# Kernel optimization log

Measured on AMD Instinct MI355X. Metric: run time of the kernel, lower is better.

## Reference

```python
import jax, jax.numpy as jnp
import numpy as np

T, B, L, I, H = 1024, 1024, 10, 10, 10


def setup_inputs() -> dict:
    key = jax.random.key(0)
    ks = jax.random.split(key, 7)
    scale = 1.0 / np.sqrt(H)
    x = jax.random.normal(ks[0], (T, B, I), dtype=jnp.float32)
    hp = jax.random.normal(ks[1], (L, B, H), dtype=jnp.float32)
    cp = jax.random.normal(ks[2], (L, B, H), dtype=jnp.float32)
    # torch nn.LSTM params, uniform(-1/sqrt(H), 1/sqrt(H)); layer 0 input = I == H so all layers stack
    W_ih = jax.random.uniform(ks[3], (L, 4 * H, I), minval=-scale, maxval=scale, dtype=jnp.float32)
    W_hh = jax.random.uniform(ks[4], (L, 4 * H, H), minval=-scale, maxval=scale, dtype=jnp.float32)
    b_ih = jax.random.uniform(ks[5], (L, 4 * H), minval=-scale, maxval=scale, dtype=jnp.float32)
    b_hh = jax.random.uniform(ks[6], (L, 4 * H), minval=-scale, maxval=scale, dtype=jnp.float32)
    return {"x": x, "hp": hp, "cp": cp, "W_ih": W_ih, "W_hh": W_hh, "b_ih": b_ih, "b_hh": b_hh}


def _run_layer(inp, h0, c0, Wi, Wh, bi, bh):
    # precompute input projections for all timesteps: [T, B, 4H]
    xg = jnp.einsum('tbi,gi->tbg', inp, Wi) + bi + bh

    def step(carry, xg_t):
        h, c = carry
        g = xg_t + h @ Wh.T  # [B, 4H]; torch gate order: i, f, g, o
        i_g, f_g, g_g, o_g = jnp.split(g, 4, axis=-1)
        i_g = jax.nn.sigmoid(i_g)
        f_g = jax.nn.sigmoid(f_g)
        g_g = jnp.tanh(g_g)
        o_g = jax.nn.sigmoid(o_g)
        c = f_g * c + i_g * g_g
        h = o_g * jnp.tanh(c)
        return (h, c), h

    (hT, cT), ys = jax.lax.scan(step, (h0, c0), xg)
    return ys, hT, cT


def reference(x, hp, cp, W_ih, W_hh, b_ih, b_hh):
    out = x
    hns, cns = [], []
    for l in range(hp.shape[0]):  # fixed small layer stack
        out, hn, cn = _run_layer(out, hp[l], cp[l], W_ih[l], W_hh[l], b_ih[l], b_hh[l])
        hns.append(hn)
        cns.append(cn)
    return out, jnp.stack(hns), jnp.stack(cns)
```

## Files before the change

kernel.cpp:

```cpp
#include <hip/hip_runtime.h>

namespace {

constexpr int T = 1024;
constexpr int B = 1024;
constexpr int L = 10;
constexpr int H = 10;
constexpr int NTHREADS = 128;
constexpr int U = 4;
constexpr int NWIN = T / U;
constexpr int NINT = NWIN + L - 1;
constexpr int BH = B * H;
constexpr int ROWP = 12;

using v2f = __attribute__((ext_vector_type(2))) float;
using v4f = __attribute__((ext_vector_type(4))) float;

__device__ __forceinline__ v2f v2fma(v2f a, v2f b, v2f c) {
    return __builtin_elementwise_fma(a, b, c);
}
__device__ __forceinline__ void pin2(v2f& v) { asm volatile("" : "+v"(v)); }
__device__ __forceinline__ float rcp_f(float x) { return __builtin_amdgcn_rcpf(x); }
__device__ __forceinline__ float exp2_f(float x) {
    float r; asm("v_exp_f32 %0, %1" : "=v"(r) : "v"(x)); return r;
}
__device__ __forceinline__ v2f lo2(v4f q) { return __builtin_shufflevector(q, q, 0, 1); }
__device__ __forceinline__ v2f hi2(v4f q) { return __builtin_shufflevector(q, q, 2, 3); }
#define LDS_FENCE asm volatile("" ::: "memory")

__global__
__attribute__((amdgpu_flat_work_group_size(NTHREADS, NTHREADS)))
__attribute__((amdgpu_waves_per_eu(2)))
void lstm_pipeline(const float* __restrict__ x,
                   const float* __restrict__ hp,
                   const float* __restrict__ cp,
                   const float* __restrict__ Wih,
                   const float* __restrict__ Whh,
                   const float* __restrict__ bih,
                   const float* __restrict__ bhh,
                   float* __restrict__ out,
                   float* __restrict__ hn,
                   float* __restrict__ cn)
{
    __shared__ __align__(16) float buf[2][U][L + 1][ROWP];

    const int tid = threadIdx.x;
    const int wv = tid >> 6;
    const int ln = tid & 63;
    int lidx;
    if (wv == 0) lidx = (ln < 60) ? ln : (ln - 10);
    else         lidx = (ln < 40) ? (60 + ln) : (90 + (ln - 40) % 10);
    const int l = lidx / 10;
    const int j = lidx % 10;
    const int b = blockIdx.x;
    const int boff = b * H + j;

    const float NL2E = -1.44269504088896340736f;
    v2f wi[4][5], wh[4][5], bias[4];
    {
        const float* WiL = Wih + (size_t)l * 4 * H * H;
        const float* WhL = Whh + (size_t)l * 4 * H * H;
        const int bo = l * 4 * H;
        #pragma unroll
        for (int g = 0; g < 4; ++g) {
            const float s = (g == 2) ? 2.0f * NL2E : NL2E;
            const float* wr = WiL + (size_t)(g * H + j) * H;
            const float* hr = WhL + (size_t)(g * H + j) * H;
            #pragma unroll
            for (int p = 0; p < 5; ++p) {
                wi[g][p][0] = wr[2 * p] * s; wi[g][p][1] = wr[2 * p + 1] * s;
                wh[g][p][0] = hr[2 * p] * s; wh[g][p][1] = hr[2 * p + 1] * s;
            }
            bias[g][0] = (bih[bo + g * H + j] + bhh[bo + g * H + j]) * s;
            bias[g][1] = 0.0f;
        }
    }
    #pragma unroll
    for (int g = 0; g < 4; ++g) {
        #pragma unroll
        for (int p = 0; p < 5; ++p) { pin2(wi[g][p]); pin2(wh[g][p]); }
        pin2(bias[g]);
    }

    float h = hp[(l * B + b) * H + j];
    float c = cp[(l * B + b) * H + j];
    buf[(l + 1) & 1][U - 1][l + 1][j] = h;

    const bool is_st = (lidx < 10);
    float xcur[U], xnext[U];
    if (is_st) {
        #pragma unroll
        for (int u = 0; u < U; ++u)
            buf[1][u][0][j] = x[(size_t)u * BH + boff];
        #pragma unroll
        for (int u = 0; u < U; ++u) xcur[u] = x[(size_t)(U + u) * BH + boff];
    }
    __syncthreads();

    v2f acc[U][4];

    auto prefetchx = [&](int k) {
        if (is_st && (k + 2) < NWIN) {
            #pragma unroll
            for (int u = 0; u < U; ++u)
                xnext[u] = x[(size_t)((k + 2) * U + u) * BH + boff];
        }
    };

    auto phase1 = [&](int k, int rp) {
        const unsigned w = (unsigned)(k - l);
        if (w < (unsigned)NWIN) {
            #pragma unroll
            for (int u = 0; u < U; ++u) {
                const float* xr = &buf[rp][u][l][0];
                v4f q0 = *(const v4f*)(xr + 0);
                v4f q1 = *(const v4f*)(xr + 4);
                v2f q2 = *(const v2f*)(xr + 8);
                #pragma unroll
                for (int g = 0; g < 4; ++g) {
                    v2f a = v2fma(wi[g][0], lo2(q0), bias[g]);
                    a = v2fma(wi[g][1], hi2(q0), a);
                    a = v2fma(wi[g][2], lo2(q1), a);
                    a = v2fma(wi[g][3], hi2(q1), a);
                    a = v2fma(wi[g][4], q2, a);
                    acc[u][g] = a;
                }
            }
        }
    };

    auto phase2 = [&](int k, int wp, int rp) {
        const unsigned w = (unsigned)(k - l);
        if (w < (unsigned)NWIN) {
            const float* hr0 = &buf[rp][U - 1][l + 1][0];
            v4f hq0 = *(const v4f*)(hr0 + 0);
            v4f hq1 = *(const v4f*)(hr0 + 4);
            v2f hq2 = *(const v2f*)(hr0 + 8);
            float hv[U];
            #pragma unroll
            for (int u = 0; u < U; ++u) {
                v4f q0, q1; v2f q2;
                if (u == 0) { q0 = hq0; q1 = hq1; q2 = hq2; }
                else {
                    const float* hr = &buf[wp][u - 1][l + 1][0];
                    q0 = *(const v4f*)(hr + 0);
                    q1 = *(const v4f*)(hr + 4);
                    q2 = *(const v2f*)(hr + 8);
                }
                v2f aI = v2fma(wh[0][0], lo2(q0), acc[u][0]);
                v2f aF = v2fma(wh[1][0], lo2(q0), acc[u][1]);
                v2f aG = v2fma(wh[2][0], lo2(q0), acc[u][2]);
                v2f aO = v2fma(wh[3][0], lo2(q0), acc[u][3]);
                aI = v2fma(wh[0][1], hi2(q0), aI);
                aF = v2fma(wh[1][1], hi2(q0), aF);
                aG = v2fma(wh[2][1], hi2(q0), aG);
                aO = v2fma(wh[3][1], hi2(q0), aO);
                aI = v2fma(wh[0][2], lo2(q1), aI);
                aF = v2fma(wh[1][2], lo2(q1), aF);
                aG = v2fma(wh[2][2], lo2(q1), aG);
                aO = v2fma(wh[3][2], lo2(q1), aO);
                aI = v2fma(wh[0][3], hi2(q1), aI);
                aF = v2fma(wh[1][3], hi2(q1), aF);
                aG = v2fma(wh[2][3], hi2(q1), aG);
                aO = v2fma(wh[3][3], hi2(q1), aO);
                aI = v2fma(wh[0][4], q2, aI);
                aF = v2fma(wh[1][4], q2, aF);
                aG = v2fma(wh[2][4], q2, aG);
                aO = v2fma(wh[3][4], q2, aO);
                const float pI = aI[0] + aI[1];
                const float pF = aF[0] + aF[1];
                const float pG = aG[0] + aG[1];
                const float pO = aO[0] + aO[1];
                const float Ei = exp2_f(pI);
                const float Ef = exp2_f(pF);
                const float Eg = exp2_f(pG);
                const float Eo = exp2_f(pO);
                const float d1 = 1.0f + Ef;
                const float e1 = 1.0f + Ei;
                const float e2 = 1.0f + Eg;
                const float d2 = e1 * e2;
                const float num = fmaf(c, d2, (1.0f - Eg) * d1);
                c = num * rcp_f(d1 * d2);
                const float Ec = exp2_f((2.0f * NL2E) * c);
                const float o1 = 1.0f + Eo;
                const float o2 = 1.0f + Ec;
                h = (1.0f - Ec) * rcp_f(o1 * o2);
                buf[wp][u][l + 1][j] = h;
                hv[u] = h;
            }
            if (l == L - 1) {
                const int t0 = (int)w * U;
                #pragma unroll
                for (int u = 0; u < U; ++u)
                    out[(size_t)(t0 + u) * BH + boff] = hv[u];
            }
        }
    };

    auto stagex = [&](int k, int wp) {
        if (is_st && (k + 1) < NWIN) {
            #pragma unroll
            for (int u = 0; u < U; ++u) buf[wp][u][0][j] = xcur[u];
            #pragma unroll
            for (int u = 0; u < U; ++u) xcur[u] = xnext[u];
        }
    };

    if (wv == 0) {
        for (int kk = 0; kk < NINT + 1; kk += 2) {
            prefetchx(kk);
            phase1(kk, 1);        LDS_FENCE;
            phase2(kk, 0, 1);     LDS_FENCE;
            stagex(kk, 0);
            __syncthreads();
            prefetchx(kk + 1);
            phase1(kk + 1, 0);    LDS_FENCE;
            phase2(kk + 1, 1, 0); LDS_FENCE;
            stagex(kk + 1, 1);
            __syncthreads();
        }
    } else {
        for (int kk = 0; kk < NINT + 1; kk += 2) {
            phase2(kk - 1, 1, 0); LDS_FENCE;
            phase1(kk, 1);
            __syncthreads();
            phase2(kk, 0, 1);     LDS_FENCE;
            phase1(kk + 1, 0);
            __syncthreads();
        }
    }

    hn[(l * B + b) * H + j] = h;
    cn[(l * B + b) * H + j] = c;
}

}

extern "C" void kernel_launch(void* const* d_in, const int* in_sizes, int n_in,
                              void* d_out, int out_size, void* d_ws, size_t ws_size,
                              hipStream_t stream) {
    (void)in_sizes; (void)n_in; (void)d_ws; (void)ws_size; (void)out_size;
    const float* x   = (const float*)d_in[0];
    const float* hp  = (const float*)d_in[1];
    const float* cp  = (const float*)d_in[2];
    const float* Wih = (const float*)d_in[3];
    const float* Whh = (const float*)d_in[4];
    const float* bih = (const float*)d_in[5];
    const float* bhh = (const float*)d_in[6];

    float* out = (float*)d_out;
    float* hn  = out + (size_t)T * B * H;
    float* cn  = hn + (size_t)L * B * H;

    lstm_pipeline<<<dim3(B), dim3(NTHREADS), 0, stream>>>(
        x, hp, cp, Wih, Whh, bih, bhh, out, hn, cn);
}
```

Baseline: 459.2 us.

## Interleave next-window input projection with recurrent steps in a fused phase

Merges the separate input-projection phase and the recurrent phase into one fused routine that computes the next window's input projection for step u-1 while doing the recurrent update for step u. The x staging store moves to the start of the fused phase, and the prefetch and buffer swap move into it. Both wavefronts now run the same fused schedule, which gives the independent phase1 FMAs a chance to fill latency gaps in the serial gate/exp chain. In exchange it adds LDS fences per step and more live registers, and the ordering of LDS reads and writes across the parity buffers becomes harder to reason about.

```diff
diff --git a/kernel.cpp b/kernel.cpp
--- a/kernel.cpp
+++ b/kernel.cpp
@@ -99,54 +99,56 @@
 
     v2f acc[U][4];
 
-    auto prefetchx = [&](int k) {
-        if (is_st && (k + 2) < NWIN) {
+    auto phase1_u = [&](int k, int par, int u) {
+        if ((unsigned)(k - l) < (unsigned)NWIN) {
+            const float* xr = &buf[par][u][l][0];
+            v4f q0 = *(const v4f*)(xr + 0);
+            v4f q1 = *(const v4f*)(xr + 4);
+            v2f q2 = *(const v2f*)(xr + 8);
+            #pragma unroll
+            for (int g = 0; g < 4; ++g) {
+                v2f a = v2fma(wi[g][0], lo2(q0), bias[g]);
+                a = v2fma(wi[g][1], hi2(q0), a);
+                a = v2fma(wi[g][2], lo2(q1), a);
+                a = v2fma(wi[g][3], hi2(q1), a);
+                a = v2fma(wi[g][4], q2, a);
+                acc[u][g] = a;
+            }
+        }
+    };
+
+    auto fused = [&](int kp2, int wp, int rp) {
+        if (is_st && (kp2 + 1) < NWIN) {
+            #pragma unroll
+            for (int u = 0; u < U; ++u) buf[wp][u][0][j] = xcur[u];
+        }
+        LDS_FENCE;
+        if (is_st && (kp2 + 2) < NWIN) {
             #pragma unroll
             for (int u = 0; u < U; ++u)
-                xnext[u] = x[(size_t)((k + 2) * U + u) * BH + boff];
-        }
-    };
-
-    auto phase1 = [&](int k, int rp) {
-        const unsigned w = (unsigned)(k - l);
-        if (w < (unsigned)NWIN) {
-            #pragma unroll
-            for (int u = 0; u < U; ++u) {
-                const float* xr = &buf[rp][u][l][0];
-                v4f q0 = *(const v4f*)(xr + 0);
-                v4f q1 = *(const v4f*)(xr + 4);
-                v2f q2 = *(const v2f*)(xr + 8);
-                #pragma unroll
-                for (int g = 0; g < 4; ++g) {
-                    v2f a = v2fma(wi[g][0], lo2(q0), bias[g]);
-                    a = v2fma(wi[g][1], hi2(q0), a);
-                    a = v2fma(wi[g][2], lo2(q1), a);
-                    a = v2fma(wi[g][3], hi2(q1), a);
-                    a = v2fma(wi[g][4], q2, a);
-                    acc[u][g] = a;
-                }
-            }
-        }
-    };
-
-    auto phase2 = [&](int k, int wp, int rp) {
-        const unsigned w = (unsigned)(k - l);
-        if (w < (unsigned)NWIN) {
+                xnext[u] = x[(size_t)((kp2 + 2) * U + u) * BH + boff];
+        }
+        const unsigned w2 = (unsigned)(kp2 - l);
+        const bool act2 = w2 < (unsigned)NWIN;
+        v4f hq0 = {}, hq1 = {}; v2f hq2 = {};
+        if (act2) {
             const float* hr0 = &buf[rp][U - 1][l + 1][0];
-            v4f hq0 = *(const v4f*)(hr0 + 0);
-            v4f hq1 = *(const v4f*)(hr0 + 4);
-            v2f hq2 = *(const v2f*)(hr0 + 8);
-            float hv[U];
-            #pragma unroll
-            for (int u = 0; u < U; ++u) {
-                v4f q0, q1; v2f q2;
-                if (u == 0) { q0 = hq0; q1 = hq1; q2 = hq2; }
-                else {
-                    const float* hr = &buf[wp][u - 1][l + 1][0];
-                    q0 = *(const v4f*)(hr + 0);
-                    q1 = *(const v4f*)(hr + 4);
-                    q2 = *(const v2f*)(hr + 8);
-                }
+            hq0 = *(const v4f*)(hr0 + 0);
+            hq1 = *(const v4f*)(hr0 + 4);
+            hq2 = *(const v2f*)(hr0 + 8);
+        }
+        float hv[U] = {};
+        #pragma unroll
+        for (int u = 0; u < U; ++u) {
+            v4f q0 = hq0, q1 = hq1; v2f q2 = hq2;
+            if (act2 && u > 0) {
+                const float* hr = &buf[wp][u - 1][l + 1][0];
+                q0 = *(const v4f*)(hr + 0);
+                q1 = *(const v4f*)(hr + 4);
+                q2 = *(const v2f*)(hr + 8);
+            }
+            if (u >= 1) phase1_u(kp2 + 1, wp, u - 1);
+            if (act2) {
                 v2f aI = v2fma(wh[0][0], lo2(q0), acc[u][0]);
                 v2f aF = v2fma(wh[1][0], lo2(q0), acc[u][1]);
                 v2f aG = v2fma(wh[2][0], lo2(q0), acc[u][2]);
@@ -188,44 +190,34 @@
                 buf[wp][u][l + 1][j] = h;
                 hv[u] = h;
             }
-            if (l == L - 1) {
-                const int t0 = (int)w * U;
-                #pragma unroll
-                for (int u = 0; u < U; ++u)
-                    out[(size_t)(t0 + u) * BH + boff] = hv[u];
-            }
+            LDS_FENCE;
+        }
+        phase1_u(kp2 + 1, wp, U - 1);
+        if (act2 && l == L - 1) {
+            const int t0 = (int)w2 * U;
+            #pragma unroll
+            for (int u = 0; u < U; ++u)
+                out[(size_t)(t0 + u) * BH + boff] = hv[u];
+        }
+        if (is_st) {
+            #pragma unroll
+            for (int u = 0; u < U; ++u) xcur[u] = xnext[u];
         }
     };
 
-    auto stagex = [&](int k, int wp) {
-        if (is_st && (k + 1) < NWIN) {
-            #pragma unroll
-            for (int u = 0; u < U; ++u) buf[wp][u][0][j] = xcur[u];
-            #pragma unroll
-            for (int u = 0; u < U; ++u) xcur[u] = xnext[u];
-        }
-    };
-
     if (wv == 0) {
+        phase1_u(0, 1, 0); phase1_u(0, 1, 1); phase1_u(0, 1, 2); phase1_u(0, 1, 3);
         for (int kk = 0; kk < NINT + 1; kk += 2) {
-            prefetchx(kk);
-            phase1(kk, 1);        LDS_FENCE;
-            phase2(kk, 0, 1);     LDS_FENCE;
-            stagex(kk, 0);
-            __syncthreads();
-            prefetchx(kk + 1);
-            phase1(kk + 1, 0);    LDS_FENCE;
-            phase2(kk + 1, 1, 0); LDS_FENCE;
-            stagex(kk + 1, 1);
+            fused(kk, 0, 1);
+            __syncthreads();
+            fused(kk + 1, 1, 0);
             __syncthreads();
         }
     } else {
         for (int kk = 0; kk < NINT + 1; kk += 2) {
-            phase2(kk - 1, 1, 0); LDS_FENCE;
-            phase1(kk, 1);
-            __syncthreads();
-            phase2(kk, 0, 1);     LDS_FENCE;
-            phase1(kk + 1, 0);
+            fused(kk - 1, 1, 0);
+            __syncthreads();
+            fused(kk, 0, 1);
             __syncthreads();
         }
     }
```

Result: slower. 528.9 us (+15.2%).
